# Kernel tuning notes

Hardware: AMD Instinct MI355X
Metric: run time of the kernel (lower is better)

Reference implementation:

```python
import jax, jax.numpy as jnp
import numpy as np

EMBED_DIM = 1024
NUM_HEADS = 16
HEAD_DIM = EMBED_DIM // NUM_HEADS


def setup_inputs() -> dict:
    key = jax.random.key(0)
    ks = jax.random.split(key, 9)
    s = 0.02
    x = jax.random.normal(ks[0], (2, 2048, EMBED_DIM), dtype=jnp.float32)
    Wq = jax.random.normal(ks[1], (EMBED_DIM, EMBED_DIM), dtype=jnp.float32) * s
    bq = jax.random.normal(ks[2], (EMBED_DIM,), dtype=jnp.float32) * s
    Wk = jax.random.normal(ks[3], (EMBED_DIM, EMBED_DIM), dtype=jnp.float32) * s
    bk = jax.random.normal(ks[4], (EMBED_DIM,), dtype=jnp.float32) * s
    Wv = jax.random.normal(ks[5], (EMBED_DIM, EMBED_DIM), dtype=jnp.float32) * s
    bv = jax.random.normal(ks[6], (EMBED_DIM,), dtype=jnp.float32) * s
    Wo = jax.random.normal(ks[7], (EMBED_DIM, EMBED_DIM), dtype=jnp.float32) * s
    bo = jax.random.normal(ks[8], (EMBED_DIM,), dtype=jnp.float32) * s
    return {"x": x, "Wq": Wq, "bq": bq, "Wk": Wk, "bk": bk,
            "Wv": Wv, "bv": bv, "Wo": Wo, "bo": bo}


def reference(x, Wq, bq, Wk, bk, Wv, bv, Wo, bo):
    B, S, E = x.shape
    H, D = NUM_HEADS, HEAD_DIM
    # torch Linear: y = x @ W.T + b, W is [out, in]
    q = (jnp.einsum('bse,fe->bsf', x, Wq) + bq).reshape(B, S, H, D).transpose(0, 2, 1, 3)
    k = (jnp.einsum('bse,fe->bsf', x, Wk) + bk).reshape(B, S, H, D).transpose(0, 2, 1, 3)
    v = (jnp.einsum('bse,fe->bsf', x, Wv) + bv).reshape(B, S, H, D).transpose(0, 2, 1, 3)
    scores = jnp.einsum('bhqd,bhkd->bhqk', q, k) / jnp.sqrt(jnp.float32(D))
    causal = jnp.triu(jnp.ones((S, S), dtype=bool), k=1)  # True above diagonal
    scores = jnp.where(causal, jnp.float32(-jnp.inf), scores)
    attn = jax.nn.softmax(scores, axis=-1)
    ctx = jnp.einsum('bhqk,bhkd->bhqd', attn, v)
    ctx = ctx.transpose(0, 2, 1, 3).reshape(B, S, E)
    out = jnp.einsum('bse,fe->bsf', ctx, Wo) + bo
    return out
```

## Files before the change

kernel.cpp:

```cpp
#include <hip/hip_runtime.h>
#include <hip/hip_bf16.h>


#define SEQ   2048
#define EMBED 1024
#define NHEADS 16
#define HDIM  64
#define MROWS 4096

typedef __attribute__((ext_vector_type(8))) short bf16x8;
typedef __attribute__((ext_vector_type(4))) float f32x4;
typedef unsigned short ush;

__device__ __forceinline__ ush bf16_rne(float x) {
    unsigned u = __builtin_bit_cast(unsigned, x);
    unsigned r = u + 0x7fffu + ((u >> 16) & 1u);
    return (ush)(r >> 16);
}
__device__ __forceinline__ float bf16_to_f32(ush h) {
    return __builtin_bit_cast(float, (unsigned)h << 16);
}

__global__ __launch_bounds__(256) void conv_hilo(
    const float* __restrict__ src, ush* __restrict__ hi, ush* __restrict__ lo,
    int n4)
{
    int i = blockIdx.x * blockDim.x + threadIdx.x;
    const int stride = gridDim.x * blockDim.x;
    for (; i < n4; i += stride) {
        const float4 v = ((const float4*)src)[i];
        ushort4 h, l;
        h.x = bf16_rne(v.x); l.x = bf16_rne(v.x - bf16_to_f32(h.x));
        h.y = bf16_rne(v.y); l.y = bf16_rne(v.y - bf16_to_f32(h.y));
        h.z = bf16_rne(v.z); l.z = bf16_rne(v.z - bf16_to_f32(h.z));
        h.w = bf16_rne(v.w); l.w = bf16_rne(v.w - bf16_to_f32(h.w));
        ((ushort4*)hi)[i] = h;
        ((ushort4*)lo)[i] = l;
    }
}

template<int OMODE>
__global__ __launch_bounds__(256) void gemm_pre(
    const ush* __restrict__ Ah_g, const ush* __restrict__ Al_g,
    const ush* __restrict__ Wh_g, const ush* __restrict__ Wl_g,
    const float* __restrict__ bias, void* __restrict__ Cv,
    int M, int N, int K)
{
    __shared__ __align__(16) ush Ah[4096];
    __shared__ __align__(16) ush Al[4096];
    __shared__ __align__(16) ush Wh[4096];
    __shared__ __align__(16) ush Wl[4096];

    const int tid = threadIdx.x;
    const int bm = blockIdx.x * 128;
    const int bn = blockIdx.y * 128;

    const int sr  = tid >> 1;
    const int kc0 = (tid & 1) * 2;

    const ush* Ap  = Ah_g + (size_t)(bm + sr) * K + kc0 * 8;
    const ush* Alp = Al_g + (size_t)(bm + sr) * K + kc0 * 8;
    const ush* Wp  = Wh_g + (size_t)(bn + sr) * K + kc0 * 8;
    const ush* Wlp = Wl_g + (size_t)(bn + sr) * K + kc0 * 8;

    const int lane = tid & 63;
    const int wv = tid >> 6;
    const int wm = (wv >> 1) * 64;
    const int wn = (wv & 1) * 64;
    const int fr = lane & 15;
    const int fk = lane >> 4;

    f32x4 acc[4][4];
    #pragma unroll
    for (int i = 0; i < 4; ++i)
        #pragma unroll
        for (int j = 0; j < 4; ++j)
            acc[i][j] = (f32x4){0.f, 0.f, 0.f, 0.f};

    bf16x8 rah[2], ral[2], rwh[2], rwl[2];
    #pragma unroll
    for (int s = 0; s < 2; ++s) {
        rah[s] = *(const bf16x8*)(Ap  + s * 8);
        ral[s] = *(const bf16x8*)(Alp + s * 8);
        rwh[s] = *(const bf16x8*)(Wp  + s * 8);
        rwl[s] = *(const bf16x8*)(Wlp + s * 8);
    }

    for (int k0 = 0; k0 < K; k0 += 32) {
        __syncthreads();

        #pragma unroll
        for (int s = 0; s < 2; ++s) {
            const int slot = ((kc0 + s) * 128 + sr) * 8;
            *(bf16x8*)&Ah[slot] = rah[s];
            *(bf16x8*)&Al[slot] = ral[s];
            *(bf16x8*)&Wh[slot] = rwh[s];
            *(bf16x8*)&Wl[slot] = rwl[s];
        }

        if (k0 + 32 < K) {
            #pragma unroll
            for (int s = 0; s < 2; ++s) {
                rah[s] = *(const bf16x8*)(Ap  + k0 + 32 + s * 8);
                ral[s] = *(const bf16x8*)(Alp + k0 + 32 + s * 8);
                rwh[s] = *(const bf16x8*)(Wp  + k0 + 32 + s * 8);
                rwl[s] = *(const bf16x8*)(Wlp + k0 + 32 + s * 8);
            }
        }

        __syncthreads();

        bf16x8 whf[4], wlf[4];
        #pragma unroll
        for (int nj = 0; nj < 4; ++nj) {
            whf[nj] = *(const bf16x8*)&Wh[(fk * 128 + wn + nj * 16 + fr) * 8];
            wlf[nj] = *(const bf16x8*)&Wl[(fk * 128 + wn + nj * 16 + fr) * 8];
        }
        #pragma unroll
        for (int mi = 0; mi < 4; ++mi) {
            const bf16x8 ah = *(const bf16x8*)&Ah[(fk * 128 + wm + mi * 16 + fr) * 8];
            const bf16x8 al = *(const bf16x8*)&Al[(fk * 128 + wm + mi * 16 + fr) * 8];
            #pragma unroll
            for (int nj = 0; nj < 4; ++nj) {
                acc[mi][nj] = __builtin_amdgcn_mfma_f32_16x16x32_bf16(ah, whf[nj], acc[mi][nj], 0, 0, 0);
                acc[mi][nj] = __builtin_amdgcn_mfma_f32_16x16x32_bf16(ah, wlf[nj], acc[mi][nj], 0, 0, 0);
                acc[mi][nj] = __builtin_amdgcn_mfma_f32_16x16x32_bf16(al, whf[nj], acc[mi][nj], 0, 0, 0);
            }
        }
    }

    #pragma unroll
    for (int mi = 0; mi < 4; ++mi) {
        const int row0 = bm + wm + mi * 16 + fk * 4;
        #pragma unroll
        for (int nj = 0; nj < 4; ++nj) {
            const int col = bn + wn + nj * 16 + fr;
            const float bb = bias[col];
            if (OMODE == 2) {
                float* cp = (float*)Cv + (size_t)row0 * N + col;
                #pragma unroll
                for (int j = 0; j < 4; ++j)
                    cp[(size_t)j * N] = acc[mi][nj][j] + bb;
            } else if (OMODE == 0) {
                ush* cp = (ush*)Cv + (size_t)row0 * N + col;
                #pragma unroll
                for (int j = 0; j < 4; ++j)
                    cp[(size_t)j * N] = bf16_rne(acc[mi][nj][j] + bb);
            } else {
                const int bb_ = row0 >> 11, s0 = row0 & 2047;
                ushort4 pk;
                pk.x = bf16_rne(acc[mi][nj][0] + bb);
                pk.y = bf16_rne(acc[mi][nj][1] + bb);
                pk.z = bf16_rne(acc[mi][nj][2] + bb);
                pk.w = bf16_rne(acc[mi][nj][3] + bb);
                *(ushort4*)((ush*)Cv + (size_t)bb_ * EMBED * SEQ
                            + (size_t)col * SEQ + s0) = pk;
            }
        }
    }
}

__global__ __launch_bounds__(256) void attn_mfma2(
    const ush* __restrict__ Qg, const ush* __restrict__ Kg,
    const ush* __restrict__ Vtg, ush* __restrict__ Oh, ush* __restrict__ Ol)
{
    __shared__ __align__(16) ush Ks[64 * 72];
    __shared__ __align__(16) ush Vs[64 * 72];
    __shared__ __align__(16) ush Ps[4][16 * 72];

    const int tid = threadIdx.x;
    const int bh = blockIdx.x;
    const int b = bh >> 4, h = bh & 15;
    const int qt = blockIdx.y;

    const int lane = tid & 63;
    const int wv = tid >> 6;
    const int fr = lane & 15;
    const int fq = lane >> 4;

    const int sr2 = tid >> 2;
    const int sc  = (tid & 3) * 16;

    const ush* qp = Qg + ((size_t)(b * SEQ + qt * 64 + wv * 16 + fr)) * EMBED
                       + h * HDIM;
    bf16x8 qf[2];
    qf[0] = *(const bf16x8*)(qp +  0 + fq * 8);
    qf[1] = *(const bf16x8*)(qp + 32 + fq * 8);

    float m_i[4], l_i[4];
    f32x4 o[4];
    #pragma unroll
    for (int r = 0; r < 4; ++r) { m_i[r] = -1e30f; l_i[r] = 0.f; }
    #pragma unroll
    for (int n = 0; n < 4; ++n) o[n] = (f32x4){0.f, 0.f, 0.f, 0.f};

    for (int kt = 0; kt <= qt; ++kt) {
        __syncthreads();

        {
            const ush* kp = Kg + ((size_t)(b * SEQ + kt * 64 + sr2)) * EMBED
                               + h * HDIM + sc;
            *(bf16x8*)&Ks[sr2 * 72 + sc]     = *(const bf16x8*)kp;
            *(bf16x8*)&Ks[sr2 * 72 + sc + 8] = *(const bf16x8*)(kp + 8);
        }
        {
            const ush* vp = Vtg + ((size_t)b * EMBED + h * HDIM + sr2) * SEQ
                                + kt * 64 + sc;
            *(bf16x8*)&Vs[sr2 * 72 + sc]     = *(const bf16x8*)vp;
            *(bf16x8*)&Vs[sr2 * 72 + sc + 8] = *(const bf16x8*)(vp + 8);
        }
        __syncthreads();

        f32x4 sc4[4];
        #pragma unroll
        for (int n = 0; n < 4; ++n) sc4[n] = (f32x4){0.f, 0.f, 0.f, 0.f};
        #pragma unroll
        for (int kc = 0; kc < 2; ++kc)
            #pragma unroll
            for (int n = 0; n < 4; ++n) {
                const bf16x8 kf = *(const bf16x8*)&Ks[(n * 16 + fr) * 72 + kc * 32 + fq * 8];
                sc4[n] = __builtin_amdgcn_mfma_f32_16x16x32_bf16(qf[kc], kf, sc4[n], 0, 0, 0);
            }

        const bool diag = (kt == qt);
        float t[4][4];
        #pragma unroll
        for (int n = 0; n < 4; ++n)
            #pragma unroll
            for (int r = 0; r < 4; ++r) {
                float s = sc4[n][r] * 0.125f;
                if (diag && (n * 16 + fr > wv * 16 + fq * 4 + r)) s = -1e30f;
                t[n][r] = s;
            }

        #pragma unroll
        for (int r = 0; r < 4; ++r) {
            float mx = fmaxf(fmaxf(t[0][r], t[1][r]), fmaxf(t[2][r], t[3][r]));
            mx = fmaxf(mx, __shfl_xor(mx, 1));
            mx = fmaxf(mx, __shfl_xor(mx, 2));
            mx = fmaxf(mx, __shfl_xor(mx, 4));
            mx = fmaxf(mx, __shfl_xor(mx, 8));
            const float mnew = fmaxf(m_i[r], mx);
            const float corr = __expf(m_i[r] - mnew);
            float ps = 0.f;
            #pragma unroll
            for (int n = 0; n < 4; ++n) {
                const float p = __expf(t[n][r] - mnew);
                Ps[wv][(fq * 4 + r) * 72 + n * 16 + fr] = bf16_rne(p);
                ps += p;
            }
            ps += __shfl_xor(ps, 1);
            ps += __shfl_xor(ps, 2);
            ps += __shfl_xor(ps, 4);
            ps += __shfl_xor(ps, 8);
            l_i[r] = l_i[r] * corr + ps;
            m_i[r] = mnew;
            o[0][r] *= corr; o[1][r] *= corr; o[2][r] *= corr; o[3][r] *= corr;
        }

        #pragma unroll
        for (int kc = 0; kc < 2; ++kc) {
            const bf16x8 pf = *(const bf16x8*)&Ps[wv][fr * 72 + kc * 32 + fq * 8];
            #pragma unroll
            for (int n = 0; n < 4; ++n) {
                const bf16x8 vf = *(const bf16x8*)&Vs[(n * 16 + fr) * 72 + kc * 32 + fq * 8];
                o[n] = __builtin_amdgcn_mfma_f32_16x16x32_bf16(pf, vf, o[n], 0, 0, 0);
            }
        }
    }

    #pragma unroll
    for (int r = 0; r < 4; ++r) {
        const float inv = 1.f / l_i[r];
        const size_t rowoff = ((size_t)(b * SEQ + qt * 64 + wv * 16 + fq * 4 + r)) * EMBED
                              + h * HDIM;
        #pragma unroll
        for (int n = 0; n < 4; ++n) {
            const float val = o[n][r] * inv;
            const ush hv = bf16_rne(val);
            Oh[rowoff + n * 16 + fr] = hv;
            Ol[rowoff + n * 16 + fr] = bf16_rne(val - bf16_to_f32(hv));
        }
    }
}

extern "C" void kernel_launch(void* const* d_in, const int* in_sizes, int n_in,
                              void* d_out, int out_size, void* d_ws, size_t ws_size,
                              hipStream_t stream)
{
    const float* x  = (const float*)d_in[0];
    const float* Wq = (const float*)d_in[1];
    const float* bq = (const float*)d_in[2];
    const float* Wk = (const float*)d_in[3];
    const float* bk = (const float*)d_in[4];
    const float* Wv = (const float*)d_in[5];
    const float* bv = (const float*)d_in[6];
    const float* Wo = (const float*)d_in[7];
    const float* bo = (const float*)d_in[8];
    float* out = (float*)d_out;

    const size_t XN = (size_t)MROWS * EMBED;
    const size_t WN = (size_t)EMBED * EMBED;
    if (ws_size < 2 * XN * sizeof(float)) return;

    ush* wsu  = (ush*)d_ws;
    ush* qb   = wsu;
    ush* kb   = wsu + XN;
    ush* x_hi = wsu + 2 * XN;
    ush* x_lo = wsu + 3 * XN;
    ush* ctx_hi = qb;
    ush* ctx_lo = x_hi;
    ush* wo_h = x_lo;
    ush* wo_l = x_lo + WN;

    ush* dov  = (ush*)d_out;
    ush* vt   = dov;
    ush* w_hi = dov + XN;
    ush* w_lo = dov + XN + WN;

    dim3 gg(MROWS / 128, EMBED / 128);

    conv_hilo<<<2048, 256, 0, stream>>>(x, x_hi, x_lo, (int)(XN / 4));

    conv_hilo<<<1024, 256, 0, stream>>>(Wq, w_hi, w_lo, (int)(WN / 4));
    gemm_pre<0><<<gg, 256, 0, stream>>>(x_hi, x_lo, w_hi, w_lo, bq, qb, MROWS, EMBED, EMBED);

    conv_hilo<<<1024, 256, 0, stream>>>(Wk, w_hi, w_lo, (int)(WN / 4));
    gemm_pre<0><<<gg, 256, 0, stream>>>(x_hi, x_lo, w_hi, w_lo, bk, kb, MROWS, EMBED, EMBED);

    conv_hilo<<<1024, 256, 0, stream>>>(Wv, w_hi, w_lo, (int)(WN / 4));
    gemm_pre<1><<<gg, 256, 0, stream>>>(x_hi, x_lo, w_hi, w_lo, bv, vt, MROWS, EMBED, EMBED);

    attn_mfma2<<<dim3(NHEADS * 2, SEQ / 64), 256, 0, stream>>>(qb, kb, vt, ctx_hi, ctx_lo);

    conv_hilo<<<1024, 256, 0, stream>>>(Wo, wo_h, wo_l, (int)(WN / 4));
    gemm_pre<2><<<gg, 256, 0, stream>>>(ctx_hi, ctx_lo, wo_h, wo_l, bo, out, MROWS, EMBED, EMBED);
}
```

Before: 313.1 us.

## Double-buffer K/V tiles, reverse tile order, and use lazy softmax rescaling

The attention kernel now double-buffers K and V tiles in shared memory, loading the next tile into registers while computing on the current one. This removes one barrier per iteration. Query tiles are launched in reverse order so the longest causal blocks start first. Softmax rescaling is skipped unless some row max grows by more than a threshold, and the row-sum reduction is deferred to the end. In exchange it uses more shared memory and registers, and the lazy max can let unnormalized exponents reach up to e^8.

```diff
diff --git a/kernel.cpp b/kernel.cpp
--- a/kernel.cpp
+++ b/kernel.cpp
@@ -160,18 +160,18 @@
     }
 }
 
-__global__ __launch_bounds__(256) void attn_mfma2(
+__global__ __launch_bounds__(256) void attn_mfma3(
     const ush* __restrict__ Qg, const ush* __restrict__ Kg,
     const ush* __restrict__ Vtg, ush* __restrict__ Oh, ush* __restrict__ Ol)
 {
-    __shared__ __align__(16) ush Ks[64 * 72];
-    __shared__ __align__(16) ush Vs[64 * 72];
+    __shared__ __align__(16) ush Ks[2][64 * 72];
+    __shared__ __align__(16) ush Vs[2][64 * 72];
     __shared__ __align__(16) ush Ps[4][16 * 72];
 
     const int tid = threadIdx.x;
     const int bh = blockIdx.x;
     const int b = bh >> 4, h = bh & 15;
-    const int qt = blockIdx.y;
+    const int qt = (SEQ / 64 - 1) - blockIdx.y;
 
     const int lane = tid & 63;
     const int wv = tid >> 6;
@@ -180,6 +180,9 @@
 
     const int sr2 = tid >> 2;
     const int sc  = (tid & 3) * 16;
+
+    const ush* kbase = Kg  + ((size_t)b * SEQ) * EMBED + h * HDIM + sc;
+    const ush* vbase = Vtg + ((size_t)b * EMBED + h * HDIM + sr2) * SEQ + sc;
 
     const ush* qp = Qg + ((size_t)(b * SEQ + qt * 64 + wv * 16 + fr)) * EMBED
                        + h * HDIM;
@@ -187,29 +190,40 @@
     qf[0] = *(const bf16x8*)(qp +  0 + fq * 8);
     qf[1] = *(const bf16x8*)(qp + 32 + fq * 8);
 
-    float m_i[4], l_i[4];
+    {
+        const ush* kp = kbase + (size_t)sr2 * EMBED;
+        const ush* vp = vbase;
+        bf16x8 k0 = *(const bf16x8*)kp;
+        bf16x8 k1 = *(const bf16x8*)(kp + 8);
+        bf16x8 v0 = *(const bf16x8*)vp;
+        bf16x8 v1 = *(const bf16x8*)(vp + 8);
+        *(bf16x8*)&Ks[0][sr2 * 72 + sc]     = k0;
+        *(bf16x8*)&Ks[0][sr2 * 72 + sc + 8] = k1;
+        *(bf16x8*)&Vs[0][sr2 * 72 + sc]     = v0;
+        *(bf16x8*)&Vs[0][sr2 * 72 + sc + 8] = v1;
+    }
+    __syncthreads();
+
+    float m_i[4], l_p[4];
     f32x4 o[4];
     #pragma unroll
-    for (int r = 0; r < 4; ++r) { m_i[r] = -1e30f; l_i[r] = 0.f; }
+    for (int r = 0; r < 4; ++r) { m_i[r] = -1e30f; l_p[r] = 0.f; }
     #pragma unroll
     for (int n = 0; n < 4; ++n) o[n] = (f32x4){0.f, 0.f, 0.f, 0.f};
 
     for (int kt = 0; kt <= qt; ++kt) {
-        __syncthreads();
-
-        {
-            const ush* kp = Kg + ((size_t)(b * SEQ + kt * 64 + sr2)) * EMBED
-                               + h * HDIM + sc;
-            *(bf16x8*)&Ks[sr2 * 72 + sc]     = *(const bf16x8*)kp;
-            *(bf16x8*)&Ks[sr2 * 72 + sc + 8] = *(const bf16x8*)(kp + 8);
-        }
-        {
-            const ush* vp = Vtg + ((size_t)b * EMBED + h * HDIM + sr2) * SEQ
-                                + kt * 64 + sc;
-            *(bf16x8*)&Vs[sr2 * 72 + sc]     = *(const bf16x8*)vp;
-            *(bf16x8*)&Vs[sr2 * 72 + sc + 8] = *(const bf16x8*)(vp + 8);
-        }
-        __syncthreads();
+        const int cur = kt & 1;
+        const bool pf = (kt < qt);
+
+        bf16x8 nk0, nk1, nv0, nv1;
+        if (pf) {
+            const ush* kp = kbase + (size_t)((kt + 1) * 64 + sr2) * EMBED;
+            const ush* vp = vbase + (kt + 1) * 64;
+            nk0 = *(const bf16x8*)kp;
+            nk1 = *(const bf16x8*)(kp + 8);
+            nv0 = *(const bf16x8*)vp;
+            nv1 = *(const bf16x8*)(vp + 8);
+        }
 
         f32x4 sc4[4];
         #pragma unroll
@@ -218,7 +232,7 @@
         for (int kc = 0; kc < 2; ++kc)
             #pragma unroll
             for (int n = 0; n < 4; ++n) {
-                const bf16x8 kf = *(const bf16x8*)&Ks[(n * 16 + fr) * 72 + kc * 32 + fq * 8];
+                const bf16x8 kf = *(const bf16x8*)&Ks[cur][(n * 16 + fr) * 72 + kc * 32 + fq * 8];
                 sc4[n] = __builtin_amdgcn_mfma_f32_16x16x32_bf16(qf[kc], kf, sc4[n], 0, 0, 0);
             }
 
@@ -233,45 +247,68 @@
                 t[n][r] = s;
             }
 
+        float pmax[4];
+        #pragma unroll
+        for (int r = 0; r < 4; ++r)
+            pmax[r] = fmaxf(fmaxf(t[0][r], t[1][r]), fmaxf(t[2][r], t[3][r]));
+
+        const bool ok = (pmax[0] <= m_i[0] + 8.f) & (pmax[1] <= m_i[1] + 8.f)
+                      & (pmax[2] <= m_i[2] + 8.f) & (pmax[3] <= m_i[3] + 8.f);
+        if (!__all(ok)) {
+            #pragma unroll
+            for (int r = 0; r < 4; ++r) {
+                float mx = pmax[r];
+                mx = fmaxf(mx, __shfl_xor(mx, 1));
+                mx = fmaxf(mx, __shfl_xor(mx, 2));
+                mx = fmaxf(mx, __shfl_xor(mx, 4));
+                mx = fmaxf(mx, __shfl_xor(mx, 8));
+                const float mnew = fmaxf(m_i[r], mx);
+                const float corr = __expf(m_i[r] - mnew);
+                l_p[r] *= corr;
+                o[0][r] *= corr; o[1][r] *= corr; o[2][r] *= corr; o[3][r] *= corr;
+                m_i[r] = mnew;
+            }
+        }
         #pragma unroll
         for (int r = 0; r < 4; ++r) {
-            float mx = fmaxf(fmaxf(t[0][r], t[1][r]), fmaxf(t[2][r], t[3][r]));
-            mx = fmaxf(mx, __shfl_xor(mx, 1));
-            mx = fmaxf(mx, __shfl_xor(mx, 2));
-            mx = fmaxf(mx, __shfl_xor(mx, 4));
-            mx = fmaxf(mx, __shfl_xor(mx, 8));
-            const float mnew = fmaxf(m_i[r], mx);
-            const float corr = __expf(m_i[r] - mnew);
             float ps = 0.f;
             #pragma unroll
             for (int n = 0; n < 4; ++n) {
-                const float p = __expf(t[n][r] - mnew);
+                const float p = __expf(t[n][r] - m_i[r]);
                 Ps[wv][(fq * 4 + r) * 72 + n * 16 + fr] = bf16_rne(p);
                 ps += p;
             }
-            ps += __shfl_xor(ps, 1);
-            ps += __shfl_xor(ps, 2);
-            ps += __shfl_xor(ps, 4);
-            ps += __shfl_xor(ps, 8);
-            l_i[r] = l_i[r] * corr + ps;
-            m_i[r] = mnew;
-            o[0][r] *= corr; o[1][r] *= corr; o[2][r] *= corr; o[3][r] *= corr;
+            l_p[r] += ps;
         }
 
         #pragma unroll
         for (int kc = 0; kc < 2; ++kc) {
-            const bf16x8 pf = *(const bf16x8*)&Ps[wv][fr * 72 + kc * 32 + fq * 8];
+            const bf16x8 pfg = *(const bf16x8*)&Ps[wv][fr * 72 + kc * 32 + fq * 8];
             #pragma unroll
             for (int n = 0; n < 4; ++n) {
-                const bf16x8 vf = *(const bf16x8*)&Vs[(n * 16 + fr) * 72 + kc * 32 + fq * 8];
-                o[n] = __builtin_amdgcn_mfma_f32_16x16x32_bf16(pf, vf, o[n], 0, 0, 0);
-            }
+                const bf16x8 vf = *(const bf16x8*)&Vs[cur][(n * 16 + fr) * 72 + kc * 32 + fq * 8];
+                o[n] = __builtin_amdgcn_mfma_f32_16x16x32_bf16(pfg, vf, o[n], 0, 0, 0);
+            }
+        }
+
+        if (pf) {
+            const int nxt = cur ^ 1;
+            *(bf16x8*)&Ks[nxt][sr2 * 72 + sc]     = nk0;
+            *(bf16x8*)&Ks[nxt][sr2 * 72 + sc + 8] = nk1;
+            *(bf16x8*)&Vs[nxt][sr2 * 72 + sc]     = nv0;
+            *(bf16x8*)&Vs[nxt][sr2 * 72 + sc + 8] = nv1;
+            __syncthreads();
         }
     }
 
     #pragma unroll
     for (int r = 0; r < 4; ++r) {
-        const float inv = 1.f / l_i[r];
+        float l = l_p[r];
+        l += __shfl_xor(l, 1);
+        l += __shfl_xor(l, 2);
+        l += __shfl_xor(l, 4);
+        l += __shfl_xor(l, 8);
+        const float inv = 1.f / l;
         const size_t rowoff = ((size_t)(b * SEQ + qt * 64 + wv * 16 + fq * 4 + r)) * EMBED
                               + h * HDIM;
         #pragma unroll
@@ -331,7 +368,7 @@
     conv_hilo<<<1024, 256, 0, stream>>>(Wv, w_hi, w_lo, (int)(WN / 4));
     gemm_pre<1><<<gg, 256, 0, stream>>>(x_hi, x_lo, w_hi, w_lo, bv, vt, MROWS, EMBED, EMBED);
 
-    attn_mfma2<<<dim3(NHEADS * 2, SEQ / 64), 256, 0, stream>>>(qb, kb, vt, ctx_hi, ctx_lo);
+    attn_mfma3<<<dim3(NHEADS * 2, SEQ / 64), 256, 0, stream>>>(qb, kb, vt, ctx_hi, ctx_lo);
 
     conv_hilo<<<1024, 256, 0, stream>>>(Wo, wo_h, wo_l, (int)(WN / 4));
     gemm_pre<2><<<gg, 256, 0, stream>>>(ctx_hi, ctx_lo, wo_h, wo_l, bo, out, MROWS, EMBED, EMBED);
```

Result: faster. 276.6 us (-11.7%).
